# Performance work log

Hardware: AMD Instinct MI355X
Metric: run time of the kernel (lower is better)

The kernel has to match this reference:

```python
import jax, jax.numpy as jnp
import numpy as np

N, E, H = 50000, 800000, 4
IN_C, HID_C, OUT_C = 128, 64, 40
NEG_SLOPE_ATT = 0.2   # PyG GATConv default
NEG_SLOPE_ACT = 0.1   # model's LeakyReLU
BN_EPS = 1e-5


def setup_inputs() -> dict:
    key = jax.random.key(0)
    ks = jax.random.split(key, 20)
    x = jax.random.normal(ks[0], (N, IN_C), dtype=jnp.float32)
    adj_m = jax.random.randint(ks[1], (2, E), 0, N, dtype=jnp.int64)
    def glorot(k, shape):
        fan = sum(shape[:2]) if len(shape) == 2 else shape[-1] * 2
        return jax.random.normal(k, shape, dtype=jnp.float32) * (2.0 / fan) ** 0.5
    W0  = glorot(ks[2], (IN_C, H * HID_C))
    as0 = glorot(ks[3], (H, HID_C)); ad0 = glorot(ks[4], (H, HID_C))
    b0  = jnp.zeros((H * HID_C,), jnp.float32)
    W1  = glorot(ks[5], (H * HID_C, H * HID_C))
    as1 = glorot(ks[6], (H, HID_C)); ad1 = glorot(ks[7], (H, HID_C))
    b1  = jnp.zeros((H * HID_C,), jnp.float32)
    # layer 2: 256 -> 40, heads averaged (concat=False)
    W2  = glorot(ks[8], (H * HID_C, H * OUT_C))
    as2 = glorot(ks[9], (H, OUT_C)); ad2 = glorot(ks[10], (H, OUT_C))
    b2  = jnp.zeros((OUT_C,), jnp.float32)
    g0 = jnp.ones((H * HID_C,), jnp.float32); be0 = jnp.zeros((H * HID_C,), jnp.float32)
    g1 = jnp.ones((H * HID_C,), jnp.float32); be1 = jnp.zeros((H * HID_C,), jnp.float32)
    return dict(x=x, adj_m=adj_m, W0=W0, as0=as0, ad0=ad0, b0=b0,
                W1=W1, as1=as1, ad1=ad1, b1=b1, W2=W2, as2=as2, ad2=ad2, b2=b2,
                g0=g0, be0=be0, g1=g1, be1=be1)


def gat_conv(x, src, dst, W, att_src, att_dst, bias, concat):
    n = x.shape[0]
    heads, out_c = att_src.shape
    h = (x @ W).reshape(n, heads, out_c)                       # [N,H,C]
    a_src = jnp.einsum('nhc,hc->nh', h, att_src)               # [N,H]
    a_dst = jnp.einsum('nhc,hc->nh', h, att_dst)
    e = jax.nn.leaky_relu(a_src[src] + a_dst[dst], NEG_SLOPE_ATT)  # [E,H]
    # segment softmax over edges grouped by destination node
    m = jax.ops.segment_max(e, dst, num_segments=n)
    m = jnp.where(jnp.isfinite(m), m, 0.0)
    ee = jnp.exp(e - m[dst])
    s = jax.ops.segment_sum(ee, dst, num_segments=n)
    alpha = ee / (s[dst] + 1e-16)                              # [E,H]
    msg = h[src] * alpha[:, :, None]                           # [E,H,C]
    out = jax.ops.segment_sum(msg, dst, num_segments=n)        # [N,H,C]
    if concat:
        return out.reshape(n, heads * out_c) + bias
    return out.mean(axis=1) + bias


def batch_norm(x, gamma, beta):
    mu = x.mean(axis=0)
    var = x.var(axis=0)
    return (x - mu) * jax.lax.rsqrt(var + BN_EPS) * gamma + beta


def reference(x, adj_m, W0, as0, ad0, b0, W1, as1, ad1, b1,
              W2, as2, ad2, b2, g0, be0, g1, be1):
    n = x.shape[0]
    loop = jnp.arange(n, dtype=adj_m.dtype)
    src = jnp.concatenate([adj_m[0], loop])   # add self-loops (PyG default)
    dst = jnp.concatenate([adj_m[1], loop])
    h = gat_conv(x, src, dst, W0, as0, ad0, b0, True)
    h = jax.nn.leaky_relu(batch_norm(h, g0, be0), NEG_SLOPE_ACT)
    h = gat_conv(h, src, dst, W1, as1, ad1, b1, True)
    h = jax.nn.leaky_relu(batch_norm(h, g1, be1), NEG_SLOPE_ACT)
    h = gat_conv(h, src, dst, W2, as2, ad2, b2, False)
    return jax.nn.log_softmax(h, axis=-1)
```

## Files before the change

### kernel.cpp

```cpp
#include <hip/hip_runtime.h>

#define NNODES 50000
#define NEDGES 800000
#define EPTOT  (NEDGES + NNODES)
#define SCAN_NB ((NNODES + 255) / 256)

typedef unsigned short u16;
typedef unsigned int   u32;
typedef __attribute__((ext_vector_type(8))) short s16x8;
typedef __attribute__((ext_vector_type(4))) float f32x4;

static __device__ __forceinline__ float lrelu(float x, float s) { return x > 0.f ? x : s * x; }
static __device__ __forceinline__ float bf2f(u16 b) { return __uint_as_float((u32)b << 16); }
static __device__ __forceinline__ u16 f2bf(float f) {
  u32 u = __float_as_uint(f);
  u32 r = (u + 0x7FFFu + ((u >> 16) & 1u)) >> 16;
  return (u16)r;
}

__device__ __forceinline__ float wred_max(float v) {
#pragma unroll
  for (int off = 32; off; off >>= 1) v = fmaxf(v, __shfl_xor(v, off));
  return v;
}
__device__ __forceinline__ float wred_sum(float v) {
#pragma unroll
  for (int off = 32; off; off >>= 1) v += __shfl_xor(v, off);
  return v;
}

__global__ void k_hist(const int* __restrict__ adj, int* __restrict__ deg) {
  int i = blockIdx.x * blockDim.x + threadIdx.x;
  if (i >= EPTOT) return;
  int d = (i < NEDGES) ? adj[NEDGES + i] : (i - NEDGES);
  atomicAdd(&deg[d], 1);
}

__global__ __launch_bounds__(256) void k_scan1(const int* __restrict__ deg,
                                               int* __restrict__ part,
                                               int* __restrict__ bsum) {
  __shared__ int sm[256];
  int t = threadIdx.x;
  int i = blockIdx.x * 256 + t;
  int v = (i < NNODES) ? deg[i] : 0;
  sm[t] = v;
  __syncthreads();
#pragma unroll
  for (int off = 1; off < 256; off <<= 1) {
    int u = (t >= off) ? sm[t - off] : 0;
    __syncthreads();
    sm[t] += u;
    __syncthreads();
  }
  if (i < NNODES) part[i] = sm[t] - v;
  if (t == 255) bsum[blockIdx.x] = sm[255];
}

__global__ __launch_bounds__(256) void k_scan2(int* __restrict__ bsum) {
  __shared__ int sm[256];
  int t = threadIdx.x;
  int v = (t < SCAN_NB) ? bsum[t] : 0;
  sm[t] = v;
  __syncthreads();
#pragma unroll
  for (int off = 1; off < 256; off <<= 1) {
    int u = (t >= off) ? sm[t - off] : 0;
    __syncthreads();
    sm[t] += u;
    __syncthreads();
  }
  if (t < SCAN_NB) bsum[t] = sm[t] - v;
}

__global__ __launch_bounds__(256) void k_scan3(const int* __restrict__ part,
                                               const int* __restrict__ bsum,
                                               int* __restrict__ rowptr,
                                               int* __restrict__ fill) {
  int i = blockIdx.x * 256 + threadIdx.x;
  if (i == 0) rowptr[NNODES] = EPTOT;
  if (i >= NNODES) return;
  int r = part[i] + bsum[blockIdx.x];
  rowptr[i] = r;
  fill[i] = r;
}

__global__ void k_fill(const int* __restrict__ adj, int* __restrict__ fill,
                       int* __restrict__ colx) {
  int i = blockIdx.x * blockDim.x + threadIdx.x;
  if (i >= EPTOT) return;
  int s, d;
  if (i < NEDGES) { s = adj[i]; d = adj[NEDGES + i]; }
  else            { s = i - NEDGES; d = s; }
  int pos = atomicAdd(&fill[d], 1);
  colx[pos] = s;
}

__global__ void k_wt(const float* __restrict__ W, u16* __restrict__ Wt, int K, int Nc) {
  int i = blockIdx.x * blockDim.x + threadIdx.x;
  if (i >= K * Nc) return;
  int n = i % Nc, k = i / Nc;
  Wt[(size_t)n * K + k] = f2bf(W[i]);
}

__global__ __launch_bounds__(256) void k_gemm_mfma(const float* __restrict__ A,
                                                   const u16* __restrict__ Wt,
                                                   u16* __restrict__ Cb,
                                                   int M, int K, int Nc) {
  __shared__ u16 As[128 * 40];
  __shared__ u16 Bs[128 * 40];
  const int tid = threadIdx.x;
  const int lane = tid & 63;
  const int wv = tid >> 6;
  const int wr = (wv >> 1) * 64, wc = (wv & 1) * 64;
  const int lr = lane & 15, lk = (lane >> 4) * 8;
  const int bm = blockIdx.x * 128, bn = blockIdx.y * 128;

  const int row0 = tid >> 2, kc0 = (tid & 3) * 8;
  const int ch1 = tid + 256;
  const int row1 = ch1 >> 2, kc1 = (ch1 & 3) * 8;

  f32x4 acc[4][4];
#pragma unroll
  for (int i = 0; i < 4; ++i)
#pragma unroll
    for (int j = 0; j < 4; ++j) {
      f32x4 z = {0.f, 0.f, 0.f, 0.f};
      acc[i][j] = z;
    }

  for (int k0 = 0; k0 < K; k0 += 32) {
    float4 a00 = {0,0,0,0}, a01 = {0,0,0,0}, a10 = {0,0,0,0}, a11 = {0,0,0,0};
    uint4 bv0 = {0,0,0,0}, bv1 = {0,0,0,0};
    {
      int ga = bm + row0;
      if (ga < M) {
        const float* p = A + (size_t)ga * K + k0 + kc0;
        a00 = *(const float4*)p; a01 = *(const float4*)(p + 4);
      }
      int gb = bn + row0;
      if (gb < Nc) bv0 = *(const uint4*)(Wt + (size_t)gb * K + k0 + kc0);
    }
    {
      int ga = bm + row1;
      if (ga < M) {
        const float* p = A + (size_t)ga * K + k0 + kc1;
        a10 = *(const float4*)p; a11 = *(const float4*)(p + 4);
      }
      int gb = bn + row1;
      if (gb < Nc) bv1 = *(const uint4*)(Wt + (size_t)gb * K + k0 + kc1);
    }
    ushort4 h00 = {f2bf(a00.x), f2bf(a00.y), f2bf(a00.z), f2bf(a00.w)};
    ushort4 h01 = {f2bf(a01.x), f2bf(a01.y), f2bf(a01.z), f2bf(a01.w)};
    ushort4 h10 = {f2bf(a10.x), f2bf(a10.y), f2bf(a10.z), f2bf(a10.w)};
    ushort4 h11 = {f2bf(a11.x), f2bf(a11.y), f2bf(a11.z), f2bf(a11.w)};

    __syncthreads();
    *(ushort4*)&As[row0 * 40 + kc0]     = h00;
    *(ushort4*)&As[row0 * 40 + kc0 + 4] = h01;
    *(ushort4*)&As[row1 * 40 + kc1]     = h10;
    *(ushort4*)&As[row1 * 40 + kc1 + 4] = h11;
    *(uint4*)&Bs[row0 * 40 + kc0] = bv0;
    *(uint4*)&Bs[row1 * 40 + kc1] = bv1;
    __syncthreads();

    s16x8 af[4], bf[4];
#pragma unroll
    for (int mi = 0; mi < 4; ++mi)
      af[mi] = *(const s16x8*)&As[(wr + mi * 16 + lr) * 40 + lk];
#pragma unroll
    for (int ni = 0; ni < 4; ++ni)
      bf[ni] = *(const s16x8*)&Bs[(wc + ni * 16 + lr) * 40 + lk];
#pragma unroll
    for (int mi = 0; mi < 4; ++mi)
#pragma unroll
      for (int ni = 0; ni < 4; ++ni)
        acc[mi][ni] = __builtin_amdgcn_mfma_f32_16x16x32_bf16(af[mi], bf[ni], acc[mi][ni], 0, 0, 0);
  }

#pragma unroll
  for (int mi = 0; mi < 4; ++mi) {
    int rowb = bm + wr + mi * 16 + (lane >> 4) * 4;
#pragma unroll
    for (int ni = 0; ni < 4; ++ni) {
      int col = bn + wc + ni * 16 + lr;
      if (col >= Nc) continue;
#pragma unroll
      for (int r = 0; r < 4; ++r) {
        int row = rowb + r;
        if (row < M) Cb[(size_t)row * Nc + col] = f2bf(acc[mi][ni][r]);
      }
    }
  }
}

__global__ __launch_bounds__(256) void k_att_hid(const u16* __restrict__ hb,
                                                 const float* __restrict__ asw,
                                                 const float* __restrict__ adw,
                                                 float* __restrict__ asrc,
                                                 float* __restrict__ adst) {
  int wid = blockIdx.x * 4 + (threadIdx.x >> 6);
  int lane = threadIdx.x & 63;
  if (wid >= NNODES) return;
  const u16* hp = hb + (size_t)wid * 256;
  float v0 = bf2f(hp[lane]), v1 = bf2f(hp[64 + lane]);
  float v2 = bf2f(hp[128 + lane]), v3 = bf2f(hp[192 + lane]);
  float ps0 = v0 * asw[lane],       pd0 = v0 * adw[lane];
  float ps1 = v1 * asw[64 + lane],  pd1 = v1 * adw[64 + lane];
  float ps2 = v2 * asw[128 + lane], pd2 = v2 * adw[128 + lane];
  float ps3 = v3 * asw[192 + lane], pd3 = v3 * adw[192 + lane];
  ps0 = wred_sum(ps0); ps1 = wred_sum(ps1); ps2 = wred_sum(ps2); ps3 = wred_sum(ps3);
  pd0 = wred_sum(pd0); pd1 = wred_sum(pd1); pd2 = wred_sum(pd2); pd3 = wred_sum(pd3);
  if (lane == 0) {
    asrc[wid * 4 + 0] = ps0; asrc[wid * 4 + 1] = ps1;
    asrc[wid * 4 + 2] = ps2; asrc[wid * 4 + 3] = ps3;
    adst[wid * 4 + 0] = pd0; adst[wid * 4 + 1] = pd1;
    adst[wid * 4 + 2] = pd2; adst[wid * 4 + 3] = pd3;
  }
}

__global__ __launch_bounds__(256) void k_att_l2(const u16* __restrict__ hb2,
                                                const float* __restrict__ asw,
                                                const float* __restrict__ adw,
                                                float* __restrict__ asrc,
                                                float* __restrict__ adst) {
  int wid = blockIdx.x * 4 + (threadIdx.x >> 6);
  int lane = threadIdx.x & 63;
  if (wid >= NNODES) return;
  const u16* hp = hb2 + (size_t)wid * 160;
  float ps0 = 0, ps1 = 0, ps2 = 0, ps3 = 0, pd0 = 0, pd1 = 0, pd2 = 0, pd3 = 0;
  if (lane < 40) {
    float v0 = bf2f(hp[lane]), v1 = bf2f(hp[40 + lane]);
    float v2 = bf2f(hp[80 + lane]), v3 = bf2f(hp[120 + lane]);
    ps0 = v0 * asw[lane];       pd0 = v0 * adw[lane];
    ps1 = v1 * asw[40 + lane];  pd1 = v1 * adw[40 + lane];
    ps2 = v2 * asw[80 + lane];  pd2 = v2 * adw[80 + lane];
    ps3 = v3 * asw[120 + lane]; pd3 = v3 * adw[120 + lane];
  }
  ps0 = wred_sum(ps0); ps1 = wred_sum(ps1); ps2 = wred_sum(ps2); ps3 = wred_sum(ps3);
  pd0 = wred_sum(pd0); pd1 = wred_sum(pd1); pd2 = wred_sum(pd2); pd3 = wred_sum(pd3);
  if (lane == 0) {
    asrc[wid * 4 + 0] = ps0; asrc[wid * 4 + 1] = ps1;
    asrc[wid * 4 + 2] = ps2; asrc[wid * 4 + 3] = ps3;
    adst[wid * 4 + 0] = pd0; adst[wid * 4 + 1] = pd1;
    adst[wid * 4 + 2] = pd2; adst[wid * 4 + 3] = pd3;
  }
}

__global__ __launch_bounds__(256) void k_aggr_hid(const u16* __restrict__ hb,
                                                  const float* __restrict__ asrc,
                                                  const float* __restrict__ adst,
                                                  const int* __restrict__ rowptr,
                                                  const int* __restrict__ colx,
                                                  const float* __restrict__ bias,
                                                  float* __restrict__ out) {
  int wid = blockIdx.x * 4 + (threadIdx.x >> 6);
  int lane = threadIdx.x & 63;
  if (wid >= NNODES) return;
  int beg = rowptr[wid], end = rowptr[wid + 1];
  float ad0 = adst[wid * 4 + 0], ad1 = adst[wid * 4 + 1];
  float ad2 = adst[wid * 4 + 2], ad3 = adst[wid * 4 + 3];

  float s0 = 0.f, s1 = 0.f, s2 = 0.f, s3 = 0.f;
  for (int i = beg + lane; i < end; i += 64) {
    int s = colx[i];
    const float* ap = asrc + (size_t)s * 4;
    s0 += expf(lrelu(ap[0] + ad0, 0.2f));
    s1 += expf(lrelu(ap[1] + ad1, 0.2f));
    s2 += expf(lrelu(ap[2] + ad2, 0.2f));
    s3 += expf(lrelu(ap[3] + ad3, 0.2f));
  }
  s0 = wred_sum(s0); s1 = wred_sum(s1); s2 = wred_sum(s2); s3 = wred_sum(s3);

  int q = lane >> 4;
  float adq = (q == 0) ? ad0 : (q == 1) ? ad1 : (q == 2) ? ad2 : ad3;
  float sq  = (q == 0) ? s0  : (q == 1) ? s1  : (q == 2) ? s2  : s3;

  float ax = 0.f, ay = 0.f, az = 0.f, aw = 0.f;
  const u16* hbl = hb + lane * 4;
  int i = beg;
  for (; i + 4 <= end; i += 4) {
    int e0 = colx[i], e1 = colx[i + 1], e2 = colx[i + 2], e3 = colx[i + 3];
    float w0 = expf(lrelu(asrc[(size_t)e0 * 4 + q] + adq, 0.2f));
    float w1 = expf(lrelu(asrc[(size_t)e1 * 4 + q] + adq, 0.2f));
    float w2 = expf(lrelu(asrc[(size_t)e2 * 4 + q] + adq, 0.2f));
    float w3 = expf(lrelu(asrc[(size_t)e3 * 4 + q] + adq, 0.2f));
    ushort4 r0 = *(const ushort4*)(hbl + (size_t)e0 * 256);
    ushort4 r1 = *(const ushort4*)(hbl + (size_t)e1 * 256);
    ushort4 r2 = *(const ushort4*)(hbl + (size_t)e2 * 256);
    ushort4 r3 = *(const ushort4*)(hbl + (size_t)e3 * 256);
    ax = fmaf(w0, bf2f(r0.x), ax); ay = fmaf(w0, bf2f(r0.y), ay);
    az = fmaf(w0, bf2f(r0.z), az); aw = fmaf(w0, bf2f(r0.w), aw);
    ax = fmaf(w1, bf2f(r1.x), ax); ay = fmaf(w1, bf2f(r1.y), ay);
    az = fmaf(w1, bf2f(r1.z), az); aw = fmaf(w1, bf2f(r1.w), aw);
    ax = fmaf(w2, bf2f(r2.x), ax); ay = fmaf(w2, bf2f(r2.y), ay);
    az = fmaf(w2, bf2f(r2.z), az); aw = fmaf(w2, bf2f(r2.w), aw);
    ax = fmaf(w3, bf2f(r3.x), ax); ay = fmaf(w3, bf2f(r3.y), ay);
    az = fmaf(w3, bf2f(r3.z), az); aw = fmaf(w3, bf2f(r3.w), aw);
  }
  for (; i < end; ++i) {
    int e0 = colx[i];
    float w0 = expf(lrelu(asrc[(size_t)e0 * 4 + q] + adq, 0.2f));
    ushort4 r0 = *(const ushort4*)(hbl + (size_t)e0 * 256);
    ax = fmaf(w0, bf2f(r0.x), ax); ay = fmaf(w0, bf2f(r0.y), ay);
    az = fmaf(w0, bf2f(r0.z), az); aw = fmaf(w0, bf2f(r0.w), aw);
  }
  float inv = 1.f / (sq + 1e-16f);
  float4 b4 = ((const float4*)bias)[lane];
  float4 o = {fmaf(ax, inv, b4.x), fmaf(ay, inv, b4.y),
              fmaf(az, inv, b4.z), fmaf(aw, inv, b4.w)};
  ((float4*)out)[(size_t)wid * 64 + lane] = o;
}

__global__ __launch_bounds__(256) void k_aggr_l2(const u16* __restrict__ hb2,
                                                 const float* __restrict__ asrc,
                                                 const float* __restrict__ adst,
                                                 const int* __restrict__ rowptr,
                                                 const int* __restrict__ colx,
                                                 const float* __restrict__ b2,
                                                 float* __restrict__ out) {
  __shared__ float tile[4][160];
  int wv = threadIdx.x >> 6;
  int wid = blockIdx.x * 4 + wv;
  int lane = threadIdx.x & 63;
  bool valid = (wid < NNODES);
  int beg = 0, end = 0;
  float ad0 = 0, ad1 = 0, ad2 = 0, ad3 = 0;
  if (valid) {
    beg = rowptr[wid]; end = rowptr[wid + 1];
    ad0 = adst[wid * 4 + 0]; ad1 = adst[wid * 4 + 1];
    ad2 = adst[wid * 4 + 2]; ad3 = adst[wid * 4 + 3];
  }
  float s0 = 0.f, s1 = 0.f, s2 = 0.f, s3 = 0.f;
  for (int i = beg + lane; i < end; i += 64) {
    int s = colx[i];
    const float* ap = asrc + (size_t)s * 4;
    s0 += expf(lrelu(ap[0] + ad0, 0.2f));
    s1 += expf(lrelu(ap[1] + ad1, 0.2f));
    s2 += expf(lrelu(ap[2] + ad2, 0.2f));
    s3 += expf(lrelu(ap[3] + ad3, 0.2f));
  }
  s0 = wred_sum(s0); s1 = wred_sum(s1); s2 = wred_sum(s2); s3 = wred_sum(s3);

  int q = lane / 10; if (q > 3) q = 3;
  float adq = (q == 0) ? ad0 : (q == 1) ? ad1 : (q == 2) ? ad2 : ad3;
  float sq  = (q == 0) ? s0  : (q == 1) ? s1  : (q == 2) ? s2  : s3;

  float ax = 0.f, ay = 0.f, az = 0.f, aw = 0.f;
  const u16* hbl = hb2 + lane * 4;
  int i = beg;
  for (; i + 4 <= end; i += 4) {
    int e0 = colx[i], e1 = colx[i + 1], e2 = colx[i + 2], e3 = colx[i + 3];
    float w0 = expf(lrelu(asrc[(size_t)e0 * 4 + q] + adq, 0.2f));
    float w1 = expf(lrelu(asrc[(size_t)e1 * 4 + q] + adq, 0.2f));
    float w2 = expf(lrelu(asrc[(size_t)e2 * 4 + q] + adq, 0.2f));
    float w3 = expf(lrelu(asrc[(size_t)e3 * 4 + q] + adq, 0.2f));
    if (lane < 40) {
      ushort4 r0 = *(const ushort4*)(hbl + (size_t)e0 * 160);
      ushort4 r1 = *(const ushort4*)(hbl + (size_t)e1 * 160);
      ushort4 r2 = *(const ushort4*)(hbl + (size_t)e2 * 160);
      ushort4 r3 = *(const ushort4*)(hbl + (size_t)e3 * 160);
      ax = fmaf(w0, bf2f(r0.x), ax); ay = fmaf(w0, bf2f(r0.y), ay);
      az = fmaf(w0, bf2f(r0.z), az); aw = fmaf(w0, bf2f(r0.w), aw);
      ax = fmaf(w1, bf2f(r1.x), ax); ay = fmaf(w1, bf2f(r1.y), ay);
      az = fmaf(w1, bf2f(r1.z), az); aw = fmaf(w1, bf2f(r1.w), aw);
      ax = fmaf(w2, bf2f(r2.x), ax); ay = fmaf(w2, bf2f(r2.y), ay);
      az = fmaf(w2, bf2f(r2.z), az); aw = fmaf(w2, bf2f(r2.w), aw);
      ax = fmaf(w3, bf2f(r3.x), ax); ay = fmaf(w3, bf2f(r3.y), ay);
      az = fmaf(w3, bf2f(r3.z), az); aw = fmaf(w3, bf2f(r3.w), aw);
    }
  }
  for (; i < end; ++i) {
    int e0 = colx[i];
    float w0 = expf(lrelu(asrc[(size_t)e0 * 4 + q] + adq, 0.2f));
    if (lane < 40) {
      ushort4 r0 = *(const ushort4*)(hbl + (size_t)e0 * 160);
      ax = fmaf(w0, bf2f(r0.x), ax); ay = fmaf(w0, bf2f(r0.y), ay);
      az = fmaf(w0, bf2f(r0.z), az); aw = fmaf(w0, bf2f(r0.w), aw);
    }
  }
  if (valid && lane < 40) {
    float inv = 1.f / (sq + 1e-16f);
    tile[wv][lane * 4 + 0] = ax * inv;
    tile[wv][lane * 4 + 1] = ay * inv;
    tile[wv][lane * 4 + 2] = az * inv;
    tile[wv][lane * 4 + 3] = aw * inv;
  }
  __syncthreads();
  int c = lane;
  float val = -3.0e38f;
  if (valid && c < 40) {
    val = 0.25f * (tile[wv][c] + tile[wv][c + 40] + tile[wv][c + 80] + tile[wv][c + 120]) + b2[c];
  }
  float mv = (valid && c < 40) ? val : -3.0e38f;
  mv = wred_max(mv);
  float ex = (valid && c < 40) ? expf(val - mv) : 0.f;
  ex = wred_sum(ex);
  if (valid && c < 40) out[(size_t)wid * 40 + c] = val - mv - logf(ex);
}

__global__ __launch_bounds__(256) void k_bnstats(const float* __restrict__ x,
                                                 float* __restrict__ stat) {
  int c = threadIdx.x;
  const int rows = (NNODES + gridDim.x - 1) / gridDim.x;
  int r0 = blockIdx.x * rows;
  int r1 = min(NNODES, r0 + rows);
  float s = 0.f, qq = 0.f;
  for (int r = r0; r < r1; ++r) {
    float v = x[(size_t)r * 256 + c];
    s += v;
    qq = fmaf(v, v, qq);
  }
  atomicAdd(&stat[c], s);
  atomicAdd(&stat[256 + c], qq);
}

__global__ void k_bnfin(const float* __restrict__ stat, const float* __restrict__ g,
                        const float* __restrict__ be, float* __restrict__ sc,
                        float* __restrict__ sh) {
  int c = threadIdx.x;
  float mean = stat[c] * (1.0f / NNODES);
  float var = stat[256 + c] * (1.0f / NNODES) - mean * mean;
  float inv = rsqrtf(var + 1e-5f);
  float a = g[c] * inv;
  sc[c] = a;
  sh[c] = be[c] - mean * a;
}

__global__ void k_bnapply(float* __restrict__ x, const float* __restrict__ sc,
                          const float* __restrict__ sh) {
  int idx = blockIdx.x * blockDim.x + threadIdx.x;
  if (idx >= NNODES * 64) return;
  float4 v = ((float4*)x)[idx];
  int cb = (idx & 63) * 4;
  v.x = lrelu(fmaf(v.x, sc[cb + 0], sh[cb + 0]), 0.1f);
  v.y = lrelu(fmaf(v.y, sc[cb + 1], sh[cb + 1]), 0.1f);
  v.z = lrelu(fmaf(v.z, sc[cb + 2], sh[cb + 2]), 0.1f);
  v.w = lrelu(fmaf(v.w, sc[cb + 3], sh[cb + 3]), 0.1f);
  ((float4*)x)[idx] = v;
}

extern "C" void kernel_launch(void* const* d_in, const int* in_sizes, int n_in,
                              void* d_out, int out_size, void* d_ws, size_t ws_size,
                              hipStream_t stream) {
  const float* x   = (const float*)d_in[0];
  const int*   adj = (const int*)d_in[1];
  const float* W0  = (const float*)d_in[2];
  const float* as0 = (const float*)d_in[3];
  const float* ad0 = (const float*)d_in[4];
  const float* b0  = (const float*)d_in[5];
  const float* W1  = (const float*)d_in[6];
  const float* as1 = (const float*)d_in[7];
  const float* ad1 = (const float*)d_in[8];
  const float* b1  = (const float*)d_in[9];
  const float* W2  = (const float*)d_in[10];
  const float* as2 = (const float*)d_in[11];
  const float* ad2 = (const float*)d_in[12];
  const float* b2  = (const float*)d_in[13];
  const float* g0  = (const float*)d_in[14];
  const float* be0 = (const float*)d_in[15];
  const float* g1  = (const float*)d_in[16];
  const float* be1 = (const float*)d_in[17];
  float* out = (float*)d_out;

  float* ws   = (float*)d_ws;
  float* bufA = ws;
  float* asrc = bufA + (size_t)NNODES * 256;
  float* adst = asrc + (size_t)NNODES * 4;
  float* stat = adst + (size_t)NNODES * 4;
  float* bnsc = stat + 512;
  float* bnsh = bnsc + 256;
  u16*   hb   = (u16*)(bnsh + 256);
  u16*   w0t  = hb + (size_t)NNODES * 256;
  u16*   w1t  = w0t + 256 * 128;
  u16*   w2t  = w1t + 256 * 256;
  int* rowptr = (int*)(w2t + 160 * 256);
  int* fill   = rowptr + (NNODES + 1);
  int* colx   = fill + NNODES;
  int* deg    = colx + EPTOT;
  int* part   = deg + NNODES;
  int* bsum   = part + NNODES;

  hipMemsetAsync(deg, 0, NNODES * sizeof(int), stream);
  k_hist<<<(EPTOT + 255) / 256, 256, 0, stream>>>(adj, deg);
  k_scan1<<<SCAN_NB, 256, 0, stream>>>(deg, part, bsum);
  k_scan2<<<1, 256, 0, stream>>>(bsum);
  k_scan3<<<SCAN_NB, 256, 0, stream>>>(part, bsum, rowptr, fill);
  k_fill<<<(EPTOT + 255) / 256, 256, 0, stream>>>(adj, fill, colx);

  k_wt<<<(128 * 256 + 255) / 256, 256, 0, stream>>>(W0, w0t, 128, 256);
  k_wt<<<(256 * 256 + 255) / 256, 256, 0, stream>>>(W1, w1t, 256, 256);
  k_wt<<<(256 * 160 + 255) / 256, 256, 0, stream>>>(W2, w2t, 256, 160);

  dim3 gg2((NNODES + 127) / 128, 2);

  k_gemm_mfma<<<gg2, 256, 0, stream>>>(x, w0t, hb, NNODES, 128, 256);
  k_att_hid<<<12500, 256, 0, stream>>>(hb, as0, ad0, asrc, adst);
  k_aggr_hid<<<12500, 256, 0, stream>>>(hb, asrc, adst, rowptr, colx, b0, bufA);
  hipMemsetAsync(stat, 0, 512 * sizeof(float), stream);
  k_bnstats<<<400, 256, 0, stream>>>(bufA, stat);
  k_bnfin<<<1, 256, 0, stream>>>(stat, g0, be0, bnsc, bnsh);
  k_bnapply<<<12500, 256, 0, stream>>>(bufA, bnsc, bnsh);

  k_gemm_mfma<<<gg2, 256, 0, stream>>>(bufA, w1t, hb, NNODES, 256, 256);
  k_att_hid<<<12500, 256, 0, stream>>>(hb, as1, ad1, asrc, adst);
  k_aggr_hid<<<12500, 256, 0, stream>>>(hb, asrc, adst, rowptr, colx, b1, bufA);
  hipMemsetAsync(stat, 0, 512 * sizeof(float), stream);
  k_bnstats<<<400, 256, 0, stream>>>(bufA, stat);
  k_bnfin<<<1, 256, 0, stream>>>(stat, g1, be1, bnsc, bnsh);
  k_bnapply<<<12500, 256, 0, stream>>>(bufA, bnsc, bnsh);

  k_gemm_mfma<<<gg2, 256, 0, stream>>>(bufA, w2t, hb, NNODES, 256, 160);
  k_att_l2<<<12500, 256, 0, stream>>>(hb, as2, ad2, asrc, adst);
  k_aggr_l2<<<12500, 256, 0, stream>>>(hb, asrc, adst, rowptr, colx, b2, out);
}
```

Before: 591.4 us.

## Fuse batch-norm apply into GEMM load and cache per-edge attention weights

Removes the separate BN-apply kernels by applying scale/shift and LeakyReLU while loading A tiles in the next layer's GEMM, avoiding a full read-write pass over the hidden activations. The aggregation kernels now store exponentiated edge logits as bf16 in a workspace array during the normalizer pass and reuse them in the message pass, replacing random asrc gathers and repeated expf. This adds an edge-sized workspace write and reduces weight precision to bf16, with a slight mismatch against the fp32 normalizer.

```diff
diff --git a/kernel.cpp b/kernel.cpp
--- a/kernel.cpp
+++ b/kernel.cpp
@@ -105,6 +105,8 @@
 __global__ __launch_bounds__(256) void k_gemm_mfma(const float* __restrict__ A,
                                                    const u16* __restrict__ Wt,
                                                    u16* __restrict__ Cb,
+                                                   const float* __restrict__ sc,
+                                                   const float* __restrict__ sh,
                                                    int M, int K, int Nc) {
   __shared__ u16 As[128 * 40];
   __shared__ u16 Bs[128 * 40];
@@ -149,6 +151,26 @@
       int gb = bn + row1;
       if (gb < Nc) bv1 = *(const uint4*)(Wt + (size_t)gb * K + k0 + kc1);
     }
+    if (sc) {
+      const float* s0p = sc + k0 + kc0; const float* h0p = sh + k0 + kc0;
+      a00.x = lrelu(fmaf(a00.x, s0p[0], h0p[0]), 0.1f);
+      a00.y = lrelu(fmaf(a00.y, s0p[1], h0p[1]), 0.1f);
+      a00.z = lrelu(fmaf(a00.z, s0p[2], h0p[2]), 0.1f);
+      a00.w = lrelu(fmaf(a00.w, s0p[3], h0p[3]), 0.1f);
+      a01.x = lrelu(fmaf(a01.x, s0p[4], h0p[4]), 0.1f);
+      a01.y = lrelu(fmaf(a01.y, s0p[5], h0p[5]), 0.1f);
+      a01.z = lrelu(fmaf(a01.z, s0p[6], h0p[6]), 0.1f);
+      a01.w = lrelu(fmaf(a01.w, s0p[7], h0p[7]), 0.1f);
+      const float* s1p = sc + k0 + kc1; const float* h1p = sh + k0 + kc1;
+      a10.x = lrelu(fmaf(a10.x, s1p[0], h1p[0]), 0.1f);
+      a10.y = lrelu(fmaf(a10.y, s1p[1], h1p[1]), 0.1f);
+      a10.z = lrelu(fmaf(a10.z, s1p[2], h1p[2]), 0.1f);
+      a10.w = lrelu(fmaf(a10.w, s1p[3], h1p[3]), 0.1f);
+      a11.x = lrelu(fmaf(a11.x, s1p[4], h1p[4]), 0.1f);
+      a11.y = lrelu(fmaf(a11.y, s1p[5], h1p[5]), 0.1f);
+      a11.z = lrelu(fmaf(a11.z, s1p[6], h1p[6]), 0.1f);
+      a11.w = lrelu(fmaf(a11.w, s1p[7], h1p[7]), 0.1f);
+    }
     ushort4 h00 = {f2bf(a00.x), f2bf(a00.y), f2bf(a00.z), f2bf(a00.w)};
     ushort4 h01 = {f2bf(a01.x), f2bf(a01.y), f2bf(a01.z), f2bf(a01.w)};
     ushort4 h10 = {f2bf(a10.x), f2bf(a10.y), f2bf(a10.z), f2bf(a10.w)};
@@ -163,18 +185,18 @@
     *(uint4*)&Bs[row1 * 40 + kc1] = bv1;
     __syncthreads();
 
-    s16x8 af[4], bf[4];
+    s16x8 af[4], bfm[4];
 #pragma unroll
     for (int mi = 0; mi < 4; ++mi)
       af[mi] = *(const s16x8*)&As[(wr + mi * 16 + lr) * 40 + lk];
 #pragma unroll
     for (int ni = 0; ni < 4; ++ni)
-      bf[ni] = *(const s16x8*)&Bs[(wc + ni * 16 + lr) * 40 + lk];
+      bfm[ni] = *(const s16x8*)&Bs[(wc + ni * 16 + lr) * 40 + lk];
 #pragma unroll
     for (int mi = 0; mi < 4; ++mi)
 #pragma unroll
       for (int ni = 0; ni < 4; ++ni)
-        acc[mi][ni] = __builtin_amdgcn_mfma_f32_16x16x32_bf16(af[mi], bf[ni], acc[mi][ni], 0, 0, 0);
+        acc[mi][ni] = __builtin_amdgcn_mfma_f32_16x16x32_bf16(af[mi], bfm[ni], acc[mi][ni], 0, 0, 0);
   }
 
 #pragma unroll
@@ -252,6 +274,7 @@
                                                   const int* __restrict__ rowptr,
                                                   const int* __restrict__ colx,
                                                   const float* __restrict__ bias,
+                                                  u16* __restrict__ ew,
                                                   float* __restrict__ out) {
   int wid = blockIdx.x * 4 + (threadIdx.x >> 6);
   int lane = threadIdx.x & 63;
@@ -264,26 +287,28 @@
   for (int i = beg + lane; i < end; i += 64) {
     int s = colx[i];
     const float* ap = asrc + (size_t)s * 4;
-    s0 += expf(lrelu(ap[0] + ad0, 0.2f));
-    s1 += expf(lrelu(ap[1] + ad1, 0.2f));
-    s2 += expf(lrelu(ap[2] + ad2, 0.2f));
-    s3 += expf(lrelu(ap[3] + ad3, 0.2f));
+    float e0 = expf(lrelu(ap[0] + ad0, 0.2f));
+    float e1 = expf(lrelu(ap[1] + ad1, 0.2f));
+    float e2 = expf(lrelu(ap[2] + ad2, 0.2f));
+    float e3 = expf(lrelu(ap[3] + ad3, 0.2f));
+    ushort4 w4 = {f2bf(e0), f2bf(e1), f2bf(e2), f2bf(e3)};
+    *(ushort4*)(ew + (size_t)i * 4) = w4;
+    s0 += e0; s1 += e1; s2 += e2; s3 += e3;
   }
   s0 = wred_sum(s0); s1 = wred_sum(s1); s2 = wred_sum(s2); s3 = wred_sum(s3);
 
   int q = lane >> 4;
-  float adq = (q == 0) ? ad0 : (q == 1) ? ad1 : (q == 2) ? ad2 : ad3;
-  float sq  = (q == 0) ? s0  : (q == 1) ? s1  : (q == 2) ? s2  : s3;
+  float sq = (q == 0) ? s0 : (q == 1) ? s1 : (q == 2) ? s2 : s3;
 
   float ax = 0.f, ay = 0.f, az = 0.f, aw = 0.f;
   const u16* hbl = hb + lane * 4;
   int i = beg;
   for (; i + 4 <= end; i += 4) {
     int e0 = colx[i], e1 = colx[i + 1], e2 = colx[i + 2], e3 = colx[i + 3];
-    float w0 = expf(lrelu(asrc[(size_t)e0 * 4 + q] + adq, 0.2f));
-    float w1 = expf(lrelu(asrc[(size_t)e1 * 4 + q] + adq, 0.2f));
-    float w2 = expf(lrelu(asrc[(size_t)e2 * 4 + q] + adq, 0.2f));
-    float w3 = expf(lrelu(asrc[(size_t)e3 * 4 + q] + adq, 0.2f));
+    float w0 = bf2f(ew[(size_t)i * 4 + q]);
+    float w1 = bf2f(ew[(size_t)(i + 1) * 4 + q]);
+    float w2 = bf2f(ew[(size_t)(i + 2) * 4 + q]);
+    float w3 = bf2f(ew[(size_t)(i + 3) * 4 + q]);
     ushort4 r0 = *(const ushort4*)(hbl + (size_t)e0 * 256);
     ushort4 r1 = *(const ushort4*)(hbl + (size_t)e1 * 256);
     ushort4 r2 = *(const ushort4*)(hbl + (size_t)e2 * 256);
@@ -299,7 +324,7 @@
   }
   for (; i < end; ++i) {
     int e0 = colx[i];
-    float w0 = expf(lrelu(asrc[(size_t)e0 * 4 + q] + adq, 0.2f));
+    float w0 = bf2f(ew[(size_t)i * 4 + q]);
     ushort4 r0 = *(const ushort4*)(hbl + (size_t)e0 * 256);
     ax = fmaf(w0, bf2f(r0.x), ax); ay = fmaf(w0, bf2f(r0.y), ay);
     az = fmaf(w0, bf2f(r0.z), az); aw = fmaf(w0, bf2f(r0.w), aw);
@@ -317,6 +342,7 @@
                                                  const int* __restrict__ rowptr,
                                                  const int* __restrict__ colx,
                                                  const float* __restrict__ b2,
+                                                 u16* __restrict__ ew,
                                                  float* __restrict__ out) {
   __shared__ float tile[4][160];
   int wv = threadIdx.x >> 6;
@@ -334,26 +360,28 @@
   for (int i = beg + lane; i < end; i += 64) {
     int s = colx[i];
     const float* ap = asrc + (size_t)s * 4;
-    s0 += expf(lrelu(ap[0] + ad0, 0.2f));
-    s1 += expf(lrelu(ap[1] + ad1, 0.2f));
-    s2 += expf(lrelu(ap[2] + ad2, 0.2f));
-    s3 += expf(lrelu(ap[3] + ad3, 0.2f));
+    float e0 = expf(lrelu(ap[0] + ad0, 0.2f));
+    float e1 = expf(lrelu(ap[1] + ad1, 0.2f));
+    float e2 = expf(lrelu(ap[2] + ad2, 0.2f));
+    float e3 = expf(lrelu(ap[3] + ad3, 0.2f));
+    ushort4 w4 = {f2bf(e0), f2bf(e1), f2bf(e2), f2bf(e3)};
+    *(ushort4*)(ew + (size_t)i * 4) = w4;
+    s0 += e0; s1 += e1; s2 += e2; s3 += e3;
   }
   s0 = wred_sum(s0); s1 = wred_sum(s1); s2 = wred_sum(s2); s3 = wred_sum(s3);
 
   int q = lane / 10; if (q > 3) q = 3;
-  float adq = (q == 0) ? ad0 : (q == 1) ? ad1 : (q == 2) ? ad2 : ad3;
-  float sq  = (q == 0) ? s0  : (q == 1) ? s1  : (q == 2) ? s2  : s3;
+  float sq = (q == 0) ? s0 : (q == 1) ? s1 : (q == 2) ? s2 : s3;
 
   float ax = 0.f, ay = 0.f, az = 0.f, aw = 0.f;
   const u16* hbl = hb2 + lane * 4;
   int i = beg;
   for (; i + 4 <= end; i += 4) {
     int e0 = colx[i], e1 = colx[i + 1], e2 = colx[i + 2], e3 = colx[i + 3];
-    float w0 = expf(lrelu(asrc[(size_t)e0 * 4 + q] + adq, 0.2f));
-    float w1 = expf(lrelu(asrc[(size_t)e1 * 4 + q] + adq, 0.2f));
-    float w2 = expf(lrelu(asrc[(size_t)e2 * 4 + q] + adq, 0.2f));
-    float w3 = expf(lrelu(asrc[(size_t)e3 * 4 + q] + adq, 0.2f));
+    float w0 = bf2f(ew[(size_t)i * 4 + q]);
+    float w1 = bf2f(ew[(size_t)(i + 1) * 4 + q]);
+    float w2 = bf2f(ew[(size_t)(i + 2) * 4 + q]);
+    float w3 = bf2f(ew[(size_t)(i + 3) * 4 + q]);
     if (lane < 40) {
       ushort4 r0 = *(const ushort4*)(hbl + (size_t)e0 * 160);
       ushort4 r1 = *(const ushort4*)(hbl + (size_t)e1 * 160);
@@ -371,7 +399,7 @@
   }
   for (; i < end; ++i) {
     int e0 = colx[i];
-    float w0 = expf(lrelu(asrc[(size_t)e0 * 4 + q] + adq, 0.2f));
+    float w0 = bf2f(ew[(size_t)i * 4 + q]);
     if (lane < 40) {
       ushort4 r0 = *(const ushort4*)(hbl + (size_t)e0 * 160);
       ax = fmaf(w0, bf2f(r0.x), ax); ay = fmaf(w0, bf2f(r0.y), ay);
@@ -424,19 +452,6 @@
   float a = g[c] * inv;
   sc[c] = a;
   sh[c] = be[c] - mean * a;
-}
-
-__global__ void k_bnapply(float* __restrict__ x, const float* __restrict__ sc,
-                          const float* __restrict__ sh) {
-  int idx = blockIdx.x * blockDim.x + threadIdx.x;
-  if (idx >= NNODES * 64) return;
-  float4 v = ((float4*)x)[idx];
-  int cb = (idx & 63) * 4;
-  v.x = lrelu(fmaf(v.x, sc[cb + 0], sh[cb + 0]), 0.1f);
-  v.y = lrelu(fmaf(v.y, sc[cb + 1], sh[cb + 1]), 0.1f);
-  v.z = lrelu(fmaf(v.z, sc[cb + 2], sh[cb + 2]), 0.1f);
-  v.w = lrelu(fmaf(v.w, sc[cb + 3], sh[cb + 3]), 0.1f);
-  ((float4*)x)[idx] = v;
 }
 
 extern "C" void kernel_launch(void* const* d_in, const int* in_sizes, int n_in,
@@ -473,7 +488,8 @@
   u16*   w0t  = hb + (size_t)NNODES * 256;
   u16*   w1t  = w0t + 256 * 128;
   u16*   w2t  = w1t + 256 * 256;
-  int* rowptr = (int*)(w2t + 160 * 256);
+  u16*   ew   = w2t + 160 * 256;
+  int* rowptr = (int*)(ew + (size_t)EPTOT * 4);
   int* fill   = rowptr + (NNODES + 1);
   int* colx   = fill + NNODES;
   int* deg    = colx + EPTOT;
@@ -493,23 +509,21 @@
 
   dim3 gg2((NNODES + 127) / 128, 2);
 
-  k_gemm_mfma<<<gg2, 256, 0, stream>>>(x, w0t, hb, NNODES, 128, 256);
+  k_gemm_mfma<<<gg2, 256, 0, stream>>>(x, w0t, hb, nullptr, nullptr, NNODES, 128, 256);
   k_att_hid<<<12500, 256, 0, stream>>>(hb, as0, ad0, asrc, adst);
-  k_aggr_hid<<<12500, 256, 0, stream>>>(hb, asrc, adst, rowptr, colx, b0, bufA);
+  k_aggr_hid<<<12500, 256, 0, stream>>>(hb, asrc, adst, rowptr, colx, b0, ew, bufA);
   hipMemsetAsync(stat, 0, 512 * sizeof(float), stream);
   k_bnstats<<<400, 256, 0, stream>>>(bufA, stat);
   k_bnfin<<<1, 256, 0, stream>>>(stat, g0, be0, bnsc, bnsh);
-  k_bnapply<<<12500, 256, 0, stream>>>(bufA, bnsc, bnsh);
-
-  k_gemm_mfma<<<gg2, 256, 0, stream>>>(bufA, w1t, hb, NNODES, 256, 256);
+
+  k_gemm_mfma<<<gg2, 256, 0, stream>>>(bufA, w1t, hb, bnsc, bnsh, NNODES, 256, 256);
   k_att_hid<<<12500, 256, 0, stream>>>(hb, as1, ad1, asrc, adst);
-  k_aggr_hid<<<12500, 256, 0, stream>>>(hb, asrc, adst, rowptr, colx, b1, bufA);
+  k_aggr_hid<<<12500, 256, 0, stream>>>(hb, asrc, adst, rowptr, colx, b1, ew, bufA);
   hipMemsetAsync(stat, 0, 512 * sizeof(float), stream);
   k_bnstats<<<400, 256, 0, stream>>>(bufA, stat);
   k_bnfin<<<1, 256, 0, stream>>>(stat, g1, be1, bnsc, bnsh);
-  k_bnapply<<<12500, 256, 0, stream>>>(bufA, bnsc, bnsh);
-
-  k_gemm_mfma<<<gg2, 256, 0, stream>>>(bufA, w2t, hb, NNODES, 256, 160);
+
+  k_gemm_mfma<<<gg2, 256, 0, stream>>>(bufA, w2t, hb, bnsc, bnsh, NNODES, 256, 160);
   k_att_l2<<<12500, 256, 0, stream>>>(hb, as2, ad2, asrc, adst);
-  k_aggr_l2<<<12500, 256, 0, stream>>>(hb, asrc, adst, rowptr, colx, b2, out);
-}
+  k_aggr_l2<<<12500, 256, 0, stream>>>(hb, asrc, adst, rowptr, colx, b2, ew, out);
+}
```

Measured after the change: 575.1 us. 1.03x faster.
